# Optimization experiments

Measured on AMD Instinct MI355X. Metric: run time of the kernel, lower is better.

The kernel has to match this reference:

```python
import jax, jax.numpy as jnp
import numpy as np

IN_FEAT = 2      # coord channels (x,y)
TH = 0.5         # threshold_relu cutoff
B, T, N = 4, 20, 256
CMAP, CC = 2048, 32   # raw / compressed visual channels
HF, WF = 16, 16       # feature-map spatial dims
IMG = 512.0           # image width/height for coord normalization
H2 = IN_FEAT * 2      # LSTM hidden = 4
H4 = IN_FEAT * 4      # Q/K/V dim = 8


def _grid_sample_local_context(fm, coords, t, n):
    """fm: (b,C,H,W); coords: (b,2,t,n) pixel coords. Bilinear grid_sample,
    align_corners=False, zero padding. Returns (b,t,n,C)."""
    b, C, H, W = fm.shape
    gx = 2.0 * (coords[:, 0].reshape(b, -1) / IMG) - 1.0  # (b,P)
    gy = 2.0 * (coords[:, 1].reshape(b, -1) / IMG) - 1.0
    ix = ((gx + 1.0) * W - 1.0) * 0.5
    iy = ((gy + 1.0) * H - 1.0) * 0.5
    x0 = jnp.floor(ix); y0 = jnp.floor(iy)
    x1 = x0 + 1.0;      y1 = y0 + 1.0
    wx1 = ix - x0; wx0 = 1.0 - wx1
    wy1 = iy - y0; wy0 = 1.0 - wy1

    def corner(xf, yf, w):
        valid = (xf >= 0) & (xf <= W - 1) & (yf >= 0) & (yf <= H - 1)
        xi = jnp.clip(xf, 0, W - 1).astype(jnp.int32)
        yi = jnp.clip(yf, 0, H - 1).astype(jnp.int32)
        vals = jax.vmap(lambda f, xx, yy: f[:, yy, xx])(fm, xi, yi)  # (b,C,P)
        return vals * (w * valid.astype(fm.dtype))[:, None, :]

    out = (corner(x0, y0, wx0 * wy0) + corner(x1, y0, wx1 * wy0)
           + corner(x0, y1, wx0 * wy1) + corner(x1, y1, wx1 * wy1))
    return jnp.transpose(out, (0, 2, 1)).reshape(b, t, n, C)


def setup_inputs() -> dict:
    key = jax.random.key(0)
    ks = jax.random.split(key, 18)
    s = 0.1
    nrm = lambda k, sh: (jax.random.normal(k, sh, jnp.float32) * s)
    return {
        "x": jax.random.uniform(ks[0], (B, 2, T, N), jnp.float32) * IMG,
        "metadata": jax.random.normal(ks[1], (B, CMAP, HF, WF), jnp.float32),
        "w_ih": nrm(ks[2], (4 * H2, IN_FEAT)),
        "b_ih": nrm(ks[3], (4 * H2,)),
        "b_hh": nrm(ks[4], (4 * H2,)),
        "comp_w": nrm(ks[5], (CC, CMAP)) * 0.1,
        "comp_b": nrm(ks[6], (CC,)),
        "vf_w": nrm(ks[7], (H2, H2 + CC)),
        "vf_b": nrm(ks[8], (H2,)),
        "fc_w": nrm(ks[9], (H4, H2)),
        "fc_b": nrm(ks[10], (H4,)),
        "fc2_w": nrm(ks[11], (H4, IN_FEAT)),
        "fc2_b": nrm(ks[12], (H4,)),
        "fc3_w": nrm(ks[13], (H4, IN_FEAT)),
        "fc3_b": nrm(ks[14], (H4,)),
        "fco_w": nrm(ks[15], (IN_FEAT, H4)),
        "fco_b": nrm(ks[16], (IN_FEAT,)),
    }


def reference(x, metadata, w_ih, b_ih, b_hh, comp_w, comp_b, vf_w, vf_b,
              fc_w, fc_b, fc2_w, fc2_b, fc3_w, fc3_b, fco_w, fco_b):
    b = x.shape[0]
    coords = x                                      # (b,2,t,n) raw pixel coords
    xp = jnp.transpose(x, (0, 2, 3, 1))             # (b,t,n,2)
    t, n = xp.shape[1], xp.shape[2]
    # positional encoding: in_feat=2 -> pe[:,0]=sin(pos), pe[:,1]=cos(pos)
    pos = jnp.arange(t, dtype=xp.dtype)
    pe = jnp.stack([jnp.sin(pos), jnp.cos(pos)], axis=-1)  # (t,2)
    xp = xp + pe[None, :, None, :]
    xr = xp.reshape(-1, IN_FEAT)                    # (b*t*n, 2)
    # single-step LSTM with h0=c0=0: gates = W_ih x + b_ih + b_hh
    gates = xr @ w_ih.T + (b_ih + b_hh)             # (B*,16)
    i_g, f_g, g_g, o_g = jnp.split(gates, 4, axis=-1)
    c = jax.nn.sigmoid(i_g) * jnp.tanh(g_g)         # c1 = i*g (c0=0)
    X = jax.nn.sigmoid(o_g) * jnp.tanh(c)           # (B*,4)
    # 1x1 conv compressor: 2048 -> 32 channels
    cm = jnp.einsum('bchw,oc->bohw', metadata, comp_w) + comp_b[None, :, None, None]
    lc = _grid_sample_local_context(cm, coords, t, n)          # (b,t,n,32)
    fused = jnp.concatenate([X, lc.reshape(X.shape[0], CC)], axis=-1)
    X = fused @ vf_w.T + vf_b                       # (B*,4)
    Q = X @ fc_w.T + fc_b                           # (B*,8)
    K = xr @ fc2_w.T + fc2_b
    V = xr @ fc3_w.T + fc3_b
    L = t * n
    Qb = Q.reshape(b, L, H4); Kb = K.reshape(b, L, H4); Vb = V.reshape(b, L, H4)
    scores = jnp.einsum('bld,bmd->blm', Qb, Kb)     # (b,L,L)
    probs = jax.nn.sigmoid(scores)                  # non-softmax attention
    outb = jnp.einsum('blm,bmd->bld', probs, Vb)    # (b,L,8)
    o = outb.reshape(-1, H4)
    o = o * (o > TH).astype(o.dtype)                # threshold_relu
    o = o @ fco_w.T + fco_b                         # (B*,2)
    return jnp.transpose(o.reshape(b, t, n, IN_FEAT), (0, 3, 1, 2))
```

## Files before the change

### kernel.cpp

```cpp
#include <hip/hip_runtime.h>
#include <math.h>

#define B_      4
#define T_      20
#define N_      256
#define L_      5120
#define CC_     32
#define CMAP_   2048
#define HW_     256
#define GRID_   1280
#define MSPLIT_ 64
#define MCHUNK_ 80
#define CSPL_   32
#define CW_     64

__device__ __forceinline__ float fexp2(float x) { return __builtin_amdgcn_exp2f(x); }
__device__ __forceinline__ float frcp(float x)  { return __builtin_amdgcn_rcpf(x); }
__device__ __forceinline__ float sigm(float x)  { return frcp(1.f + fexp2(-1.44269504f * x)); }
__device__ __forceinline__ float tanh_(float x) { return 1.f - 2.f * frcp(fexp2(2.88539008f * x) + 1.f); }

__device__ __forceinline__ void st_f1(float* p, float a) {
    __hip_atomic_store((unsigned*)p, __float_as_uint(a),
                       __ATOMIC_RELAXED, __HIP_MEMORY_SCOPE_AGENT);
}
__device__ __forceinline__ float ld_f1(const float* p) {
    return __uint_as_float(__hip_atomic_load((const unsigned*)p,
                       __ATOMIC_RELAXED, __HIP_MEMORY_SCOPE_AGENT));
}
__device__ __forceinline__ void st_f2(float* p, float a, float b) {
    union { float f[2]; unsigned long long u; } v; v.f[0] = a; v.f[1] = b;
    __hip_atomic_store((unsigned long long*)p, v.u,
                       __ATOMIC_RELAXED, __HIP_MEMORY_SCOPE_AGENT);
}
__device__ __forceinline__ float2 ld_f2(const float* p) {
    union { float f[2]; unsigned long long u; } v;
    v.u = __hip_atomic_load((const unsigned long long*)p,
                       __ATOMIC_RELAXED, __HIP_MEMORY_SCOPE_AGENT);
    return make_float2(v.f[0], v.f[1]);
}

__device__ __forceinline__ void gbar(unsigned* cnt, unsigned* gen, unsigned my_g) {
    __syncthreads();
    if (threadIdx.x == 0) {
        int grp = blockIdx.x >> 6;
        unsigned prev = __hip_atomic_fetch_add(&cnt[grp * 16], 1u,
                                               __ATOMIC_RELAXED, __HIP_MEMORY_SCOPE_AGENT);
        if (prev == 64u * (my_g + 1u) - 1u) {
            unsigned pr = __hip_atomic_fetch_add(&cnt[32 * 16], 1u,
                                                 __ATOMIC_RELAXED, __HIP_MEMORY_SCOPE_AGENT);
            if (pr == 20u * (my_g + 1u) - 1u) {
                __hip_atomic_store(gen, my_g + 1u, __ATOMIC_RELAXED, __HIP_MEMORY_SCOPE_AGENT);
            } else {
                while (__hip_atomic_load(gen, __ATOMIC_RELAXED, __HIP_MEMORY_SCOPE_AGENT) < my_g + 1u)
                    __builtin_amdgcn_s_sleep(32);
            }
        } else {
            while (__hip_atomic_load(gen, __ATOMIC_RELAXED, __HIP_MEMORY_SCOPE_AGENT) < my_g + 1u)
                __builtin_amdgcn_s_sleep(32);
        }
    }
    __syncthreads();
}


__global__ void __launch_bounds__(256, 5) k_fused(
        const float* __restrict__ x,      const float* __restrict__ md,
        const float* __restrict__ w_ih,   const float* __restrict__ b_ih,
        const float* __restrict__ b_hh,
        const float* __restrict__ comp_w, const float* __restrict__ comp_b,
        const float* __restrict__ vf_w,   const float* __restrict__ vf_b,
        const float* __restrict__ fc_w,   const float* __restrict__ fc_b,
        const float* __restrict__ fc2_w,  const float* __restrict__ fc2_b,
        const float* __restrict__ fc3_w,  const float* __restrict__ fc3_b,
        const float* __restrict__ fco_w,  const float* __restrict__ fco_b,
        float* __restrict__ ws, float* __restrict__ out) {
    __shared__ float xs[2 * MCHUNK_];
    unsigned* cnt = (unsigned*)ws;
    unsigned* gen = cnt + 33 * 16;
    float* pcm  = ws + 1152;
    float* cm   = pcm + CSPL_ * B_ * CC_ * HW_;
    float* ABC  = cm + B_ * CC_ * HW_;
    float* XM   = ABC + 4 * B_ * L_;
    float* part = XM + 2 * B_ * L_;

    int blk = blockIdx.x, tid = threadIdx.x;

    if (blk < B_ * CSPL_) {
        int cs = blk & (CSPL_ - 1);
        int b  = blk >> 5;
        int c0 = cs * CW_;
        const float* mp = md + ((size_t)(b * CMAP_ + c0)) * HW_ + tid;
        const float* wp = comp_w + c0;
        float a[CC_];
        #pragma unroll
        for (int o = 0; o < CC_; ++o) a[o] = 0.f;
        for (int cc = 0; cc < CW_; ++cc) {
            float mv = mp[(size_t)cc * HW_];
            #pragma unroll
            for (int o = 0; o < CC_; ++o)
                a[o] = fmaf(wp[o * CMAP_ + cc], mv, a[o]);
        }
        float* pp = pcm + (size_t)(cs * B_ + b) * (CC_ * HW_) + tid;
        #pragma unroll
        for (int o = 0; o < CC_; ++o) st_f1(pp + o * HW_, a[o]);
    }
    gbar(cnt, gen, 0u);

    if (blk < 128) {
        int i = blk * 256 + tid;
        float s = comp_b[(i >> 8) & 31];
        #pragma unroll
        for (int ps = 0; ps < CSPL_; ++ps) s += ld_f1(pcm + ps * (B_ * CC_ * HW_) + i);
        st_f1(cm + i, s);
    }
    gbar(cnt, gen, 1u);

    if (blk < 80) {
        int p = blk * 256 + tid;
        int b = p / L_;
        int l = p - b * L_;
        int t = l >> 8, n = l & 255;
        float x0r = x[((b * 2 + 0) * T_ + t) * N_ + n];
        float x1r = x[((b * 2 + 1) * T_ + t) * N_ + n];
        float xr0 = x0r + sinf((float)t);
        float xr1 = x1r + cosf((float)t);
        float Xh[4];
        #pragma unroll
        for (int k = 0; k < 4; ++k) {
            float ig = w_ih[(k)      * 2] * xr0 + w_ih[(k)      * 2 + 1] * xr1 + b_ih[k]      + b_hh[k];
            float gg = w_ih[(8 + k)  * 2] * xr0 + w_ih[(8 + k)  * 2 + 1] * xr1 + b_ih[8 + k]  + b_hh[8 + k];
            float og = w_ih[(12 + k) * 2] * xr0 + w_ih[(12 + k) * 2 + 1] * xr1 + b_ih[12 + k] + b_hh[12 + k];
            float c = sigm(ig) * tanh_(gg);
            Xh[k] = sigm(og) * tanh_(c);
        }
        float ix = x0r * 0.03125f - 0.5f;
        float iy = x1r * 0.03125f - 0.5f;
        float x0f = floorf(ix), y0f = floorf(iy);
        float wx1 = ix - x0f, wx0 = 1.f - wx1;
        float wy1 = iy - y0f, wy0 = 1.f - wy1;
        int x0 = (int)x0f, y0 = (int)y0f;
        int x1 = x0 + 1, y1 = y0 + 1;
        bool vx0 = (x0 >= 0) && (x0 <= 15), vx1 = (x1 >= 0) && (x1 <= 15);
        bool vy0 = (y0 >= 0) && (y0 <= 15), vy1 = (y1 >= 0) && (y1 <= 15);
        int cx0 = min(max(x0, 0), 15), cx1 = min(max(x1, 0), 15);
        int cy0 = min(max(y0, 0), 15), cy1 = min(max(y1, 0), 15);
        float wg0 = (vx0 && vy0) ? wx0 * wy0 : 0.f; int of0 = cy0 * 16 + cx0;
        float wg1 = (vx1 && vy0) ? wx1 * wy0 : 0.f; int of1 = cy0 * 16 + cx1;
        float wg2 = (vx0 && vy1) ? wx0 * wy1 : 0.f; int of2 = cy1 * 16 + cx0;
        float wg3 = (vx1 && vy1) ? wx1 * wy1 : 0.f; int of3 = cy1 * 16 + cx1;
        float X2[4];
        #pragma unroll
        for (int j = 0; j < 4; ++j)
            X2[j] = vf_b[j] + vf_w[j * 36 + 0] * Xh[0] + vf_w[j * 36 + 1] * Xh[1]
                            + vf_w[j * 36 + 2] * Xh[2] + vf_w[j * 36 + 3] * Xh[3];
        const float* cmb = cm + (size_t)b * CC_ * HW_;
        #pragma unroll 8
        for (int c = 0; c < 32; ++c) {
            const float* pch = cmb + c * HW_;
            float lc = wg0 * ld_f1(pch + of0) + wg1 * ld_f1(pch + of1)
                     + wg2 * ld_f1(pch + of2) + wg3 * ld_f1(pch + of3);
            #pragma unroll
            for (int j = 0; j < 4; ++j) X2[j] += vf_w[j * 36 + 4 + c] * lc;
        }
        float A = 0.f, Bv = 0.f, C = 0.f;
        #pragma unroll
        for (int j = 0; j < 8; ++j) {
            float Qj = fc_b[j] + fc_w[j * 4 + 0] * X2[0] + fc_w[j * 4 + 1] * X2[1]
                               + fc_w[j * 4 + 2] * X2[2] + fc_w[j * 4 + 3] * X2[3];
            A  += Qj * fc2_w[j * 2 + 0];
            Bv += Qj * fc2_w[j * 2 + 1];
            C  += Qj * fc2_b[j];
        }
        const float NLG2E = -1.44269504f;
        st_f2(ABC + 4 * (size_t)p,     NLG2E * A, NLG2E * Bv);
        st_f2(ABC + 4 * (size_t)p + 2, NLG2E * C, 0.f);
        st_f2(XM  + 2 * (size_t)p,     xr0, xr1);
    }
    gbar(cnt, gen, 2u);

    {
        int ms = blk & (MSPLIT_ - 1);
        int rest = blk >> 6;
        int lt = rest % 5, b = rest / 5;
        if (tid < MCHUNK_) {
            float2 v = ld_f2(XM + 2 * ((size_t)b * L_ + ms * MCHUNK_ + tid));
            xs[2 * tid] = v.x; xs[2 * tid + 1] = v.y;
        }
        float A[4], Bv[4], C[4], S0[4], S1[4], Sp[4];
        #pragma unroll
        for (int k = 0; k < 4; ++k) {
            int l = lt * 1024 + k * 256 + tid;
            float2 ab = ld_f2(ABC + 4 * ((size_t)b * L_ + l));
            float2 cz = ld_f2(ABC + 4 * ((size_t)b * L_ + l) + 2);
            A[k] = ab.x; Bv[k] = ab.y; C[k] = cz.x;
            S0[k] = 0.f; S1[k] = 0.f; Sp[k] = 0.f;
        }
        __syncthreads();
        #pragma unroll 4
        for (int j = 0; j < MCHUNK_; ++j) {
            float x0 = xs[2 * j], x1 = xs[2 * j + 1];
            #pragma unroll
            for (int k = 0; k < 4; ++k) {
                float e = fexp2(fmaf(A[k], x0, fmaf(Bv[k], x1, C[k])));
                float pb = frcp(1.f + e);
                S0[k] = fmaf(pb, x0, S0[k]);
                S1[k] = fmaf(pb, x1, S1[k]);
                Sp[k] += pb;
            }
        }
        #pragma unroll
        for (int k = 0; k < 4; ++k) {
            int l = lt * 1024 + k * 256 + tid;
            float* pr = part + 4 * ((size_t)(ms * B_ + b) * L_ + l);
            st_f2(pr,     S0[k], S1[k]);
            st_f2(pr + 2, Sp[k], 0.f);
        }
    }
    gbar(cnt, gen, 3u);

    if (blk < 80) {
        int p = blk * 256 + tid;
        int b = p / L_, l = p - b * L_;
        float s0 = 0.f, s1 = 0.f, sp = 0.f;
        for (int s = 0; s < MSPLIT_; ++s) {
            const float* pr = part + 4 * ((size_t)(s * B_ + b) * L_ + l);
            float2 u = ld_f2(pr);
            float2 v = ld_f2(pr + 2);
            s0 += u.x; s1 += u.y; sp += v.x;
        }
        float o0 = fco_b[0], o1 = fco_b[1];
        #pragma unroll
        for (int d = 0; d < 8; ++d) {
            float od = fc3_w[d * 2 + 0] * s0 + fc3_w[d * 2 + 1] * s1 + fc3_b[d] * sp;
            od = od > 0.5f ? od : 0.f;
            o0 += fco_w[d] * od;
            o1 += fco_w[8 + d] * od;
        }
        int t = l >> 8, n = l & 255;
        out[((b * 2 + 0) * T_ + t) * N_ + n] = o0;
        out[((b * 2 + 1) * T_ + t) * N_ + n] = o1;
    }
}

extern "C" void kernel_launch(void* const* d_in, const int* in_sizes, int n_in,
                              void* d_out, int out_size, void* d_ws, size_t ws_size,
                              hipStream_t stream) {
    const float* x      = (const float*)d_in[0];
    const float* md     = (const float*)d_in[1];
    const float* w_ih   = (const float*)d_in[2];
    const float* b_ih   = (const float*)d_in[3];
    const float* b_hh   = (const float*)d_in[4];
    const float* comp_w = (const float*)d_in[5];
    const float* comp_b = (const float*)d_in[6];
    const float* vf_w   = (const float*)d_in[7];
    const float* vf_b   = (const float*)d_in[8];
    const float* fc_w   = (const float*)d_in[9];
    const float* fc_b   = (const float*)d_in[10];
    const float* fc2_w  = (const float*)d_in[11];
    const float* fc2_b  = (const float*)d_in[12];
    const float* fc3_w  = (const float*)d_in[13];
    const float* fc3_b  = (const float*)d_in[14];
    const float* fco_w  = (const float*)d_in[15];
    const float* fco_b  = (const float*)d_in[16];

    hipMemsetAsync(d_ws, 0, 4608, stream);
    hipLaunchKernelGGL(k_fused, dim3(GRID_), dim3(256), 0, stream,
                       x, md, w_ih, b_ih, b_hh, comp_w, comp_b,
                       vf_w, vf_b, fc_w, fc_b, fc2_w, fc2_b,
                       fc3_w, fc3_b, fco_w, fco_b,
                       (float*)d_ws, (float*)d_out);
}
```

Baseline: 179.9 us.

## Replace compressor partial-sum pass with atomics, drop a grid barrier, split final reduction

The 1x1-conv compressor now accumulates its partial sums straight into a channel-last cm buffer with float atomic adds. This removes the separate reduction phase and one grid-wide barrier, and the bias is folded into the bilinear gather through the weight sum. The gather reads two channels per load from the new layout. The final 64-way reduction is split across 4 threads per point with a shared-memory combine, and the barrier tree uses groups of 32 blocks with a shorter sleep. The cost is a larger memset to zero the accumulation buffer, plus atomic contention from 32 blocks adding into the same locations.

```diff
diff --git a/kernel.cpp b/kernel.cpp
--- a/kernel.cpp
+++ b/kernel.cpp
@@ -19,14 +19,6 @@
 __device__ __forceinline__ float sigm(float x)  { return frcp(1.f + fexp2(-1.44269504f * x)); }
 __device__ __forceinline__ float tanh_(float x) { return 1.f - 2.f * frcp(fexp2(2.88539008f * x) + 1.f); }
 
-__device__ __forceinline__ void st_f1(float* p, float a) {
-    __hip_atomic_store((unsigned*)p, __float_as_uint(a),
-                       __ATOMIC_RELAXED, __HIP_MEMORY_SCOPE_AGENT);
-}
-__device__ __forceinline__ float ld_f1(const float* p) {
-    return __uint_as_float(__hip_atomic_load((const unsigned*)p,
-                       __ATOMIC_RELAXED, __HIP_MEMORY_SCOPE_AGENT));
-}
 __device__ __forceinline__ void st_f2(float* p, float a, float b) {
     union { float f[2]; unsigned long long u; } v; v.f[0] = a; v.f[1] = b;
     __hip_atomic_store((unsigned long long*)p, v.u,
@@ -42,21 +34,21 @@
 __device__ __forceinline__ void gbar(unsigned* cnt, unsigned* gen, unsigned my_g) {
     __syncthreads();
     if (threadIdx.x == 0) {
-        int grp = blockIdx.x >> 6;
+        int grp = blockIdx.x >> 5;
         unsigned prev = __hip_atomic_fetch_add(&cnt[grp * 16], 1u,
                                                __ATOMIC_RELAXED, __HIP_MEMORY_SCOPE_AGENT);
-        if (prev == 64u * (my_g + 1u) - 1u) {
-            unsigned pr = __hip_atomic_fetch_add(&cnt[32 * 16], 1u,
+        if (prev == 32u * (my_g + 1u) - 1u) {
+            unsigned pr = __hip_atomic_fetch_add(&cnt[40 * 16], 1u,
                                                  __ATOMIC_RELAXED, __HIP_MEMORY_SCOPE_AGENT);
-            if (pr == 20u * (my_g + 1u) - 1u) {
+            if (pr == 40u * (my_g + 1u) - 1u) {
                 __hip_atomic_store(gen, my_g + 1u, __ATOMIC_RELAXED, __HIP_MEMORY_SCOPE_AGENT);
             } else {
                 while (__hip_atomic_load(gen, __ATOMIC_RELAXED, __HIP_MEMORY_SCOPE_AGENT) < my_g + 1u)
-                    __builtin_amdgcn_s_sleep(32);
+                    __builtin_amdgcn_s_sleep(8);
             }
         } else {
             while (__hip_atomic_load(gen, __ATOMIC_RELAXED, __HIP_MEMORY_SCOPE_AGENT) < my_g + 1u)
-                __builtin_amdgcn_s_sleep(32);
+                __builtin_amdgcn_s_sleep(8);
         }
     }
     __syncthreads();
@@ -75,13 +67,13 @@
         const float* __restrict__ fco_w,  const float* __restrict__ fco_b,
         float* __restrict__ ws, float* __restrict__ out) {
     __shared__ float xs[2 * MCHUNK_];
+    __shared__ float rs[256 * 3];
     unsigned* cnt = (unsigned*)ws;
-    unsigned* gen = cnt + 33 * 16;
-    float* pcm  = ws + 1152;
-    float* cm   = pcm + CSPL_ * B_ * CC_ * HW_;
-    float* ABC  = cm + B_ * CC_ * HW_;
-    float* XM   = ABC + 4 * B_ * L_;
-    float* part = XM + 2 * B_ * L_;
+    unsigned* gen = cnt + 41 * 16;
+    float* cm   = ws + 672;
+    float* ABC  = ws + 33440;
+    float* XM   = ws + 115360;
+    float* part = ws + 156320;
 
     int blk = blockIdx.x, tid = threadIdx.x;
 
@@ -100,20 +92,11 @@
             for (int o = 0; o < CC_; ++o)
                 a[o] = fmaf(wp[o * CMAP_ + cc], mv, a[o]);
         }
-        float* pp = pcm + (size_t)(cs * B_ + b) * (CC_ * HW_) + tid;
-        #pragma unroll
-        for (int o = 0; o < CC_; ++o) st_f1(pp + o * HW_, a[o]);
+        float* cp = cm + ((size_t)b * HW_ + tid) * CC_;
+        #pragma unroll
+        for (int o = 0; o < CC_; ++o) unsafeAtomicAdd(cp + o, a[o]);
     }
     gbar(cnt, gen, 0u);
-
-    if (blk < 128) {
-        int i = blk * 256 + tid;
-        float s = comp_b[(i >> 8) & 31];
-        #pragma unroll
-        for (int ps = 0; ps < CSPL_; ++ps) s += ld_f1(pcm + ps * (B_ * CC_ * HW_) + i);
-        st_f1(cm + i, s);
-    }
-    gbar(cnt, gen, 1u);
 
     if (blk < 80) {
         int p = blk * 256 + tid;
@@ -148,19 +131,31 @@
         float wg1 = (vx1 && vy0) ? wx1 * wy0 : 0.f; int of1 = cy0 * 16 + cx1;
         float wg2 = (vx0 && vy1) ? wx0 * wy1 : 0.f; int of2 = cy1 * 16 + cx0;
         float wg3 = (vx1 && vy1) ? wx1 * wy1 : 0.f; int of3 = cy1 * 16 + cx1;
+        float wsum = wg0 + wg1 + wg2 + wg3;
         float X2[4];
         #pragma unroll
         for (int j = 0; j < 4; ++j)
             X2[j] = vf_b[j] + vf_w[j * 36 + 0] * Xh[0] + vf_w[j * 36 + 1] * Xh[1]
                             + vf_w[j * 36 + 2] * Xh[2] + vf_w[j * 36 + 3] * Xh[3];
-        const float* cmb = cm + (size_t)b * CC_ * HW_;
-        #pragma unroll 8
-        for (int c = 0; c < 32; ++c) {
-            const float* pch = cmb + c * HW_;
-            float lc = wg0 * ld_f1(pch + of0) + wg1 * ld_f1(pch + of1)
-                     + wg2 * ld_f1(pch + of2) + wg3 * ld_f1(pch + of3);
-            #pragma unroll
-            for (int j = 0; j < 4; ++j) X2[j] += vf_w[j * 36 + 4 + c] * lc;
+        const float* cmb = cm + (size_t)b * HW_ * CC_;
+        const float* p0 = cmb + of0 * CC_;
+        const float* p1 = cmb + of1 * CC_;
+        const float* p2 = cmb + of2 * CC_;
+        const float* p3 = cmb + of3 * CC_;
+        #pragma unroll 4
+        for (int cp2 = 0; cp2 < 16; ++cp2) {
+            float2 v0 = ld_f2(p0 + 2 * cp2);
+            float2 v1 = ld_f2(p1 + 2 * cp2);
+            float2 v2 = ld_f2(p2 + 2 * cp2);
+            float2 v3 = ld_f2(p3 + 2 * cp2);
+            float lcA = wg0 * v0.x + wg1 * v1.x + wg2 * v2.x + wg3 * v3.x
+                      + comp_b[2 * cp2] * wsum;
+            float lcB = wg0 * v0.y + wg1 * v1.y + wg2 * v2.y + wg3 * v3.y
+                      + comp_b[2 * cp2 + 1] * wsum;
+            #pragma unroll
+            for (int j = 0; j < 4; ++j)
+                X2[j] += vf_w[j * 36 + 4 + 2 * cp2] * lcA
+                       + vf_w[j * 36 + 5 + 2 * cp2] * lcB;
         }
         float A = 0.f, Bv = 0.f, C = 0.f;
         #pragma unroll
@@ -176,7 +171,7 @@
         st_f2(ABC + 4 * (size_t)p + 2, NLG2E * C, 0.f);
         st_f2(XM  + 2 * (size_t)p,     xr0, xr1);
     }
-    gbar(cnt, gen, 2u);
+    gbar(cnt, gen, 1u);
 
     {
         int ms = blk & (MSPLIT_ - 1);
@@ -216,29 +211,41 @@
             st_f2(pr + 2, Sp[k], 0.f);
         }
     }
-    gbar(cnt, gen, 3u);
-
-    if (blk < 80) {
-        int p = blk * 256 + tid;
+    gbar(cnt, gen, 2u);
+
+    if (blk < 320) {
+        int idx = blk * 256 + tid;
+        int p = idx >> 2, sub = idx & 3;
         int b = p / L_, l = p - b * L_;
         float s0 = 0.f, s1 = 0.f, sp = 0.f;
-        for (int s = 0; s < MSPLIT_; ++s) {
+        #pragma unroll 4
+        for (int s = sub * 16; s < sub * 16 + 16; ++s) {
             const float* pr = part + 4 * ((size_t)(s * B_ + b) * L_ + l);
             float2 u = ld_f2(pr);
             float2 v = ld_f2(pr + 2);
             s0 += u.x; s1 += u.y; sp += v.x;
         }
-        float o0 = fco_b[0], o1 = fco_b[1];
-        #pragma unroll
-        for (int d = 0; d < 8; ++d) {
-            float od = fc3_w[d * 2 + 0] * s0 + fc3_w[d * 2 + 1] * s1 + fc3_b[d] * sp;
-            od = od > 0.5f ? od : 0.f;
-            o0 += fco_w[d] * od;
-            o1 += fco_w[8 + d] * od;
-        }
-        int t = l >> 8, n = l & 255;
-        out[((b * 2 + 0) * T_ + t) * N_ + n] = o0;
-        out[((b * 2 + 1) * T_ + t) * N_ + n] = o1;
+        rs[tid * 3 + 0] = s0; rs[tid * 3 + 1] = s1; rs[tid * 3 + 2] = sp;
+        __syncthreads();
+        if (sub == 0) {
+            #pragma unroll
+            for (int q = 1; q < 4; ++q) {
+                s0 += rs[(tid + q) * 3 + 0];
+                s1 += rs[(tid + q) * 3 + 1];
+                sp += rs[(tid + q) * 3 + 2];
+            }
+            float o0 = fco_b[0], o1 = fco_b[1];
+            #pragma unroll
+            for (int d = 0; d < 8; ++d) {
+                float od = fc3_w[d * 2 + 0] * s0 + fc3_w[d * 2 + 1] * s1 + fc3_b[d] * sp;
+                od = od > 0.5f ? od : 0.f;
+                o0 += fco_w[d] * od;
+                o1 += fco_w[8 + d] * od;
+            }
+            int t = l >> 8, n = l & 255;
+            out[((b * 2 + 0) * T_ + t) * N_ + n] = o0;
+            out[((b * 2 + 1) * T_ + t) * N_ + n] = o1;
+        }
     }
 }
 
@@ -263,7 +270,7 @@
     const float* fco_w  = (const float*)d_in[15];
     const float* fco_b  = (const float*)d_in[16];
 
-    hipMemsetAsync(d_ws, 0, 4608, stream);
+    hipMemsetAsync(d_ws, 0, 133760, stream);
     hipLaunchKernelGGL(k_fused, dim3(GRID_), dim3(256), 0, stream,
                        x, md, w_ih, b_ih, b_hh, comp_w, comp_b,
                        vf_w, vf_b, fc_w, fc_b, fc2_w, fc2_b,
```

Measured after the change: 236.3 us. 31.4% more time.
